# Kernel optimization log

Hardware: AMD Instinct MI355X
Metric: run time of the kernel (lower is better)

The kernel has to match this reference:

```python
import jax, jax.numpy as jnp
import numpy as np

N_HEAD = 16

def setup_inputs() -> dict:
    key = jax.random.key(0)
    k1, k2, k3 = jax.random.split(key, 3)
    B, S, D = 2, 2048, 1024
    std = 0.02
    return {
        "hidden_states": jax.random.normal(k1, (B, S, D), jnp.float32),
        "w_attn": jax.random.normal(k2, (D, 3 * D), jnp.float32) * std,
        "b_attn": jnp.zeros((3 * D,), jnp.float32),
        "w_proj": jax.random.normal(k3, (D, D), jnp.float32) * std,
        "b_proj": jnp.zeros((D,), jnp.float32),
    }

def reference(hidden_states, w_attn, b_attn, w_proj, b_proj):
    B, S, D = hidden_states.shape
    H = N_HEAD
    hd = D // H
    # fused qkv projection (Conv1D == x @ W + b)
    qkv = hidden_states @ w_attn + b_attn            # [B,S,3D]
    q, k, v = jnp.split(qkv, 3, axis=-1)
    def split_heads(t):
        return t.reshape(B, S, H, hd).transpose(0, 2, 1, 3)  # [B,H,S,hd]
    q, k, v = split_heads(q), split_heads(k), split_heads(v)
    # scores with scale = sqrt(head_dim)
    scores = jnp.einsum('bhqd,bhkd->bhqk', q, k) / jnp.sqrt(jnp.asarray(hd, q.dtype))
    causal = jnp.tril(jnp.ones((S, S), bool))
    mask_value = jnp.finfo(scores.dtype).min
    scores = jnp.where(causal, scores, mask_value)
    attn = jax.nn.softmax(scores, axis=-1)           # dropout p=0 (eval)
    out = jnp.einsum('bhqk,bhkd->bhqd', attn, v)     # [B,H,S,hd]
    out = out.transpose(0, 2, 1, 3).reshape(B, S, D)
    out = out @ w_proj + b_proj
    return out
```

## Files before the change

### kernel.cpp

```cpp
#include <hip/hip_runtime.h>

#define S_LEN 2048
#define D_MODEL 1024
#define NHEAD 16
#define HDIM 64
#define BATCH 2
#define M_ROWS (BATCH * S_LEN)
#define N_QKV (3 * D_MODEL)
#define QSCALE 0.18033688011112042f

typedef __attribute__((ext_vector_type(8))) short bf16x8;
typedef __attribute__((ext_vector_type(4))) float f32x4;

static __device__ __forceinline__ unsigned short f2bf(float f) {
  unsigned int u = __float_as_uint(f);
  u += 0x7FFFu + ((u >> 16) & 1u);
  return (unsigned short)(u >> 16);
}
static __device__ __forceinline__ unsigned int pkbf(float a, float b) {
  unsigned int ua = __float_as_uint(a) + 0x8000u;
  unsigned int ub = __float_as_uint(b) + 0x8000u;
  return __builtin_amdgcn_perm(ub, ua, 0x07060302u);
}

static __device__ __forceinline__ void async_cp16(unsigned short* lds, const unsigned short* g) {
  __builtin_amdgcn_global_load_lds((__attribute__((address_space(1))) void*)g,
                                   (__attribute__((address_space(3))) void*)lds, 16, 0, 0);
}

__global__ __launch_bounds__(256) void k_prep(const float* __restrict__ x,
                                              unsigned short* __restrict__ xb,
                                              const float* __restrict__ w_attn,
                                              unsigned short* __restrict__ wqkvT,
                                              const float* __restrict__ w_proj,
                                              unsigned short* __restrict__ wprojT) {
  __shared__ unsigned short T[32][33];
  const int blk = blockIdx.x;
  const int tid = threadIdx.x;
  if (blk < 4096) {
    int i = blk * 256 + tid;
    float4 v = ((const float4*)x)[i];
    ushort4 o;
    o.x = f2bf(v.x); o.y = f2bf(v.y); o.z = f2bf(v.z); o.w = f2bf(v.w);
    ((ushort4*)xb)[i] = o;
    return;
  }
  const float* w;
  unsigned short* wT;
  int bid, Ndim;
  if (blk < 7168) { bid = blk - 4096; w = w_attn; wT = wqkvT; Ndim = N_QKV; }
  else            { bid = blk - 7168; w = w_proj; wT = wprojT; Ndim = D_MODEL; }
  const int nb = Ndim / 32;
  const int n0 = (bid % nb) * 32, k0 = (bid / nb) * 32;
  const int tx = tid & 31, ty = tid >> 5;
#pragma unroll
  for (int j = 0; j < 4; ++j) {
    int r = ty + j * 8;
    T[r][tx] = f2bf(w[(size_t)(k0 + r) * Ndim + n0 + tx]);
  }
  __syncthreads();
#pragma unroll
  for (int j = 0; j < 4; ++j) {
    int r = ty + j * 8;
    wT[(size_t)(n0 + r) * D_MODEL + k0 + tx] = T[tx][r];
  }
}

__global__ __launch_bounds__(256) void k_gemm_qkv(const unsigned short* __restrict__ A,
                                                  const unsigned short* __restrict__ Bt,
                                                  const float* __restrict__ bias,
                                                  unsigned short* __restrict__ Qb,
                                                  unsigned short* __restrict__ Kbuf,
                                                  unsigned short* __restrict__ VTb) {
  __shared__ __align__(16) unsigned short As[2][128 * 32];
  __shared__ __align__(16) unsigned short Bs[2][128 * 32];
  const int tid = threadIdx.x;
  const int wid = tid >> 6, lane = tid & 63;
  const int lr = lane & 15, lg = lane >> 4;
  const int blk = blockIdx.x;
  const int xcd = blk & 7, idx = blk >> 3;
  const int bm = ((xcd & 3) * 8 + (idx & 7)) * 128;
  const int bn = ((xcd >> 2) * 12 + (idx >> 3)) * 128;
  const int wm = (wid >> 1) * 64, wn = (wid & 1) * 64;
  const int K = D_MODEL;
  const int c0 = tid, c1 = tid + 256;
  const size_t a0o = (size_t)(bm + (c0 >> 2)) * K + (c0 & 3) * 8;
  const size_t a1o = (size_t)(bm + (c1 >> 2)) * K + (c1 & 3) * 8;
  const size_t b0o = (size_t)(bn + (c0 >> 2)) * K + (c0 & 3) * 8;
  const size_t b1o = (size_t)(bn + (c1 >> 2)) * K + (c1 & 3) * 8;

  f32x4 acc[4][4] = {};

  async_cp16(&As[0][c0 * 8], &A[a0o]);
  async_cp16(&As[0][c1 * 8], &A[a1o]);
  async_cp16(&Bs[0][c0 * 8], &Bt[b0o]);
  async_cp16(&Bs[0][c1 * 8], &Bt[b1o]);

  for (int k0 = 0; k0 < K; k0 += 32) {
    const int p = (k0 >> 5) & 1;
    __syncthreads();
    if (k0 + 32 < K) {
      async_cp16(&As[p ^ 1][c0 * 8], &A[a0o + k0 + 32]);
      async_cp16(&As[p ^ 1][c1 * 8], &A[a1o + k0 + 32]);
      async_cp16(&Bs[p ^ 1][c0 * 8], &Bt[b0o + k0 + 32]);
      async_cp16(&Bs[p ^ 1][c1 * 8], &Bt[b1o + k0 + 32]);
    }
    bf16x8 af[4], bfr[4];
#pragma unroll
    for (int i = 0; i < 4; ++i) af[i] = *(const bf16x8*)&As[p][(wm + i * 16 + lr) * 32 + lg * 8];
#pragma unroll
    for (int t = 0; t < 4; ++t) bfr[t] = *(const bf16x8*)&Bs[p][(wn + t * 16 + lr) * 32 + lg * 8];
#pragma unroll
    for (int i = 0; i < 4; ++i)
#pragma unroll
      for (int t = 0; t < 4; ++t)
        acc[i][t] = __builtin_amdgcn_mfma_f32_16x16x32_bf16(af[i], bfr[t], acc[i][t], 0, 0, 0);
  }
#pragma unroll
  for (int i = 0; i < 4; ++i) {
#pragma unroll
    for (int t = 0; t < 4; ++t) {
      int n = bn + wn + t * 16 + lr;
      int part = n >> 10, rem = n & 1023;
      int h = rem >> 6, d = rem & 63;
      float bv = bias[n];
      int row0 = bm + wm + i * 16 + lg * 4;
      int bb = row0 >> 11, s0 = row0 & 2047;
      if (part == 2) {
        ushort4 vv;
        vv.x = f2bf(acc[i][t][0] + bv);
        vv.y = f2bf(acc[i][t][1] + bv);
        vv.z = f2bf(acc[i][t][2] + bv);
        vv.w = f2bf(acc[i][t][3] + bv);
        *(ushort4*)&VTb[(((size_t)(bb << 4) + h) * HDIM + d) * S_LEN + s0] = vv;
      } else {
        unsigned short* dst = (part == 0) ? Qb : Kbuf;
        float sc = (part == 0) ? QSCALE : 1.0f;
#pragma unroll
        for (int r = 0; r < 4; ++r)
          dst[(((size_t)(bb << 4) + h) * S_LEN + (s0 + r)) * HDIM + d] = f2bf((acc[i][t][r] + bv) * sc);
      }
    }
  }
}

__global__ __launch_bounds__(256) void k_gemm_proj(const unsigned short* __restrict__ A,
                                                   const unsigned short* __restrict__ Bt,
                                                   const float* __restrict__ bias,
                                                   float* __restrict__ out) {
  __shared__ __align__(16) unsigned short As[2][128 * 32];
  __shared__ __align__(16) unsigned short Bs[2][128 * 32];
  const int tid = threadIdx.x;
  const int wid = tid >> 6, lane = tid & 63;
  const int lr = lane & 15, lg = lane >> 4;
  const int blk = blockIdx.x;
  const int xcd = blk & 7, idx = blk >> 3;
  const int bm = (xcd * 4 + (idx & 3)) * 128;
  const int bn = (idx >> 2) * 128;
  const int wm = (wid >> 1) * 64, wn = (wid & 1) * 64;
  const int K = D_MODEL;
  const int c0 = tid, c1 = tid + 256;
  const size_t a0o = (size_t)(bm + (c0 >> 2)) * K + (c0 & 3) * 8;
  const size_t a1o = (size_t)(bm + (c1 >> 2)) * K + (c1 & 3) * 8;
  const size_t b0o = (size_t)(bn + (c0 >> 2)) * K + (c0 & 3) * 8;
  const size_t b1o = (size_t)(bn + (c1 >> 2)) * K + (c1 & 3) * 8;

  f32x4 acc[4][4] = {};

  async_cp16(&As[0][c0 * 8], &A[a0o]);
  async_cp16(&As[0][c1 * 8], &A[a1o]);
  async_cp16(&Bs[0][c0 * 8], &Bt[b0o]);
  async_cp16(&Bs[0][c1 * 8], &Bt[b1o]);

  for (int k0 = 0; k0 < K; k0 += 32) {
    const int p = (k0 >> 5) & 1;
    __syncthreads();
    if (k0 + 32 < K) {
      async_cp16(&As[p ^ 1][c0 * 8], &A[a0o + k0 + 32]);
      async_cp16(&As[p ^ 1][c1 * 8], &A[a1o + k0 + 32]);
      async_cp16(&Bs[p ^ 1][c0 * 8], &Bt[b0o + k0 + 32]);
      async_cp16(&Bs[p ^ 1][c1 * 8], &Bt[b1o + k0 + 32]);
    }
    bf16x8 af[4], bfr[4];
#pragma unroll
    for (int i = 0; i < 4; ++i) af[i] = *(const bf16x8*)&As[p][(wm + i * 16 + lr) * 32 + lg * 8];
#pragma unroll
    for (int t = 0; t < 4; ++t) bfr[t] = *(const bf16x8*)&Bs[p][(wn + t * 16 + lr) * 32 + lg * 8];
#pragma unroll
    for (int i = 0; i < 4; ++i)
#pragma unroll
      for (int t = 0; t < 4; ++t)
        acc[i][t] = __builtin_amdgcn_mfma_f32_16x16x32_bf16(af[i], bfr[t], acc[i][t], 0, 0, 0);
  }
#pragma unroll
  for (int i = 0; i < 4; ++i) {
#pragma unroll
    for (int t = 0; t < 4; ++t) {
      int n = bn + wn + t * 16 + lr;
      float bv = bias[n];
#pragma unroll
      for (int r = 0; r < 4; ++r) {
        int row = bm + wm + i * 16 + lg * 4 + r;
        out[(size_t)row * D_MODEL + n] = acc[i][t][r] + bv;
      }
    }
  }
}

__global__ __launch_bounds__(256, 2) void k_attn6(const unsigned short* __restrict__ Qb,
                                                  const unsigned short* __restrict__ Kb,
                                                  const unsigned short* __restrict__ VT,
                                                  unsigned short* __restrict__ AO) {
  const int tid = threadIdx.x;
  const int wid = tid >> 6, lane = tid & 63;
  const int lr = lane & 15, quad = lane >> 4;
  const int bh = blockIdx.x;
  const int slot = blockIdx.y;
  const int b = bh >> 4, h = bh & 15;

  __shared__ __align__(16) unsigned short Ks[64 * 64];
  __shared__ __align__(16) unsigned short Vs[64 * 64];
  __shared__ __align__(16) unsigned short Pbuf[4][16 * 72];
  unsigned short* pb = &Pbuf[wid][0];

  const unsigned short* Kbh = Kb + (size_t)bh * S_LEN * HDIM;
  const unsigned short* VTbh = VT + (size_t)bh * HDIM * S_LEN;

  const int sL = slot * 4 + wid;
  const int Rs[2] = {sL * 16, (127 - sL) * 16};
  const int ntile = ((127 - slot * 4) >> 2) + 1;

  bf16x8 qf[2][2];
#pragma unroll
  for (int st = 0; st < 2; ++st)
#pragma unroll
    for (int dh = 0; dh < 2; ++dh)
      qf[st][dh] = *(const bf16x8*)&Qb[((size_t)bh * S_LEN + Rs[st] + lr) * HDIM + dh * 32 + quad * 8];

  f32x4 Ot[2][4] = {};
  float ms[2] = {-1e30f, -1e30f};
  float ls[2] = {0.f, 0.f};

  const int srow = lane >> 3;
  const int scol = ((lane & 7) ^ srow) * 8;

  for (int kt = 0; kt < ntile; ++kt) {
    const int k0 = kt * 64;
    __syncthreads();
#pragma unroll
    for (int j = 0; j < 2; ++j) {
      const int r0 = wid * 16 + j * 8;
      async_cp16(&Ks[r0 * 64 + lane * 8], &Kbh[(size_t)(k0 + r0 + srow) * HDIM + scol]);
      async_cp16(&Vs[r0 * 64 + lane * 8], &VTbh[(size_t)(r0 + srow) * S_LEN + k0 + scol]);
    }
    __syncthreads();

    bf16x8 kf[4][2], vf[4][2];
#pragma unroll
    for (int kg = 0; kg < 4; ++kg)
#pragma unroll
      for (int dh = 0; dh < 2; ++dh)
        kf[kg][dh] = *(const bf16x8*)&Ks[(kg * 16 + lr) * 64 + (((dh * 4 + quad) ^ (lr & 7)) * 8)];
#pragma unroll
    for (int dg = 0; dg < 4; ++dg)
#pragma unroll
      for (int kh = 0; kh < 2; ++kh)
        vf[dg][kh] = *(const bf16x8*)&Vs[(dg * 16 + lr) * 64 + (((kh * 4 + quad) ^ (lr & 7)) * 8)];

#pragma unroll
    for (int st = 0; st < 2; ++st) {
      const int R = Rs[st];
      if (k0 > R + 15) continue;
      f32x4 Sv[4];
#pragma unroll
      for (int kg = 0; kg < 4; ++kg) {
        f32x4 a = {};
        a = __builtin_amdgcn_mfma_f32_16x16x32_bf16(kf[kg][0], qf[st][0], a, 0, 0, 0);
        a = __builtin_amdgcn_mfma_f32_16x16x32_bf16(kf[kg][1], qf[st][1], a, 0, 0, 0);
        Sv[kg] = a;
      }
      if (k0 + 63 > R) {
        const int q = R + lr;
#pragma unroll
        for (int kg = 0; kg < 4; ++kg)
#pragma unroll
          for (int r = 0; r < 4; ++r)
            if (k0 + kg * 16 + quad * 4 + r > q) Sv[kg][r] = -1e30f;
      }
      float mx = ms[st];
#pragma unroll
      for (int kg = 0; kg < 4; ++kg)
        mx = fmaxf(mx, fmaxf(fmaxf(Sv[kg][0], Sv[kg][1]), fmaxf(Sv[kg][2], Sv[kg][3])));
      mx = fmaxf(mx, __shfl_xor(mx, 16));
      mx = fmaxf(mx, __shfl_xor(mx, 32));
      const float alpha = __builtin_amdgcn_exp2f(ms[st] - mx);
      ms[st] = mx;
      float rs = 0.f;
#pragma unroll
      for (int kg = 0; kg < 4; ++kg) {
        float e0 = __builtin_amdgcn_exp2f(Sv[kg][0] - mx);
        float e1 = __builtin_amdgcn_exp2f(Sv[kg][1] - mx);
        float e2 = __builtin_amdgcn_exp2f(Sv[kg][2] - mx);
        float e3 = __builtin_amdgcn_exp2f(Sv[kg][3] - mx);
        rs += (e0 + e1) + (e2 + e3);
        *(unsigned int*)&pb[lr * 72 + kg * 16 + quad * 4]     = pkbf(e0, e1);
        *(unsigned int*)&pb[lr * 72 + kg * 16 + quad * 4 + 2] = pkbf(e2, e3);
      }
      rs += __shfl_xor(rs, 16);
      rs += __shfl_xor(rs, 32);
      ls[st] = ls[st] * alpha + rs;
#pragma unroll
      for (int dg = 0; dg < 4; ++dg)
#pragma unroll
        for (int r = 0; r < 4; ++r) Ot[st][dg][r] *= alpha;
      bf16x8 pf0 = *(const bf16x8*)&pb[lr * 72 + quad * 8];
      bf16x8 pf1 = *(const bf16x8*)&pb[lr * 72 + 32 + quad * 8];
#pragma unroll
      for (int dg = 0; dg < 4; ++dg) {
        Ot[st][dg] = __builtin_amdgcn_mfma_f32_16x16x32_bf16(vf[dg][0], pf0, Ot[st][dg], 0, 0, 0);
        Ot[st][dg] = __builtin_amdgcn_mfma_f32_16x16x32_bf16(vf[dg][1], pf1, Ot[st][dg], 0, 0, 0);
      }
    }
  }

#pragma unroll
  for (int st = 0; st < 2; ++st) {
    const float rl = __builtin_amdgcn_rcpf(ls[st]);
    const int s = Rs[st] + lr;
#pragma unroll
    for (int dg = 0; dg < 4; ++dg) {
      const size_t o = ((size_t)b * S_LEN + s) * D_MODEL + h * 64 + dg * 16 + quad * 4;
      *(unsigned int*)&AO[o]     = pkbf(Ot[st][dg][0] * rl, Ot[st][dg][1] * rl);
      *(unsigned int*)&AO[o + 2] = pkbf(Ot[st][dg][2] * rl, Ot[st][dg][3] * rl);
    }
  }
}

extern "C" void kernel_launch(void* const* d_in, const int* in_sizes, int n_in,
                              void* d_out, int out_size, void* d_ws, size_t ws_size,
                              hipStream_t stream) {
  const float* x      = (const float*)d_in[0];
  const float* w_attn = (const float*)d_in[1];
  const float* b_attn = (const float*)d_in[2];
  const float* w_proj = (const float*)d_in[3];
  const float* b_proj = (const float*)d_in[4];
  float* out = (float*)d_out;

  unsigned short* ws     = (unsigned short*)d_ws;
  unsigned short* xb     = ws;
  unsigned short* wqkvT  = xb + (size_t)M_ROWS * D_MODEL;
  unsigned short* wprojT = wqkvT + (size_t)N_QKV * D_MODEL;
  unsigned short* Qb     = wprojT + (size_t)D_MODEL * D_MODEL;
  unsigned short* Kb     = Qb + (size_t)M_ROWS * D_MODEL;
  unsigned short* VT     = Kb + (size_t)M_ROWS * D_MODEL;
  unsigned short* AO     = xb;

  k_prep<<<8192, 256, 0, stream>>>(x, xb, w_attn, wqkvT, w_proj, wprojT);
  k_gemm_qkv<<<768, 256, 0, stream>>>(xb, wqkvT, b_attn, Qb, Kb, VT);
  k_attn6<<<dim3(BATCH * NHEAD, 16), 256, 0, stream>>>(Qb, Kb, VT, AO);
  k_gemm_proj<<<256, 256, 0, stream>>>(AO, wprojT, b_proj, out);
}
```

Baseline: 179.9 us.

## Double-buffer K/V tiles in attention and flatten grid with reordered slots

The attention kernel now keeps two LDS buffers for the K and V tiles. It prefetches the next tile with async copies while computing on the current one, replacing the load-then-barrier pattern that stalled each iteration. The 2D grid becomes a 1D grid, with the work-slot order reversed for the second half of blocks, to change how uneven causal work is scheduled across CUs. LDS use per block roughly doubles for K/V. Overlap depends on the compiler not inserting conservative waits on the outstanding LDS-targeted loads.

```diff
diff --git a/kernel.cpp b/kernel.cpp
--- a/kernel.cpp
+++ b/kernel.cpp
@@ -207,19 +207,21 @@
   }
 }
 
-__global__ __launch_bounds__(256, 2) void k_attn6(const unsigned short* __restrict__ Qb,
+__global__ __launch_bounds__(256, 2) void k_attn7(const unsigned short* __restrict__ Qb,
                                                   const unsigned short* __restrict__ Kb,
                                                   const unsigned short* __restrict__ VT,
                                                   unsigned short* __restrict__ AO) {
   const int tid = threadIdx.x;
   const int wid = tid >> 6, lane = tid & 63;
   const int lr = lane & 15, quad = lane >> 4;
-  const int bh = blockIdx.x;
-  const int slot = blockIdx.y;
+  const int blk = blockIdx.x;
+  const int bh = blk & 31;
+  const int g = blk >> 5;
+  const int slot = (g < 8) ? g : 23 - g;
   const int b = bh >> 4, h = bh & 15;
 
-  __shared__ __align__(16) unsigned short Ks[64 * 64];
-  __shared__ __align__(16) unsigned short Vs[64 * 64];
+  __shared__ __align__(16) unsigned short Ks[2][64 * 64];
+  __shared__ __align__(16) unsigned short Vs[2][64 * 64];
   __shared__ __align__(16) unsigned short Pbuf[4][16 * 72];
   unsigned short* pb = &Pbuf[wid][0];
 
@@ -244,28 +246,38 @@
   const int srow = lane >> 3;
   const int scol = ((lane & 7) ^ srow) * 8;
 
+#pragma unroll
+  for (int j = 0; j < 2; ++j) {
+    const int r0 = wid * 16 + j * 8;
+    async_cp16(&Ks[0][r0 * 64 + lane * 8], &Kbh[(size_t)(r0 + srow) * HDIM + scol]);
+    async_cp16(&Vs[0][r0 * 64 + lane * 8], &VTbh[(size_t)(r0 + srow) * S_LEN + scol]);
+  }
+
   for (int kt = 0; kt < ntile; ++kt) {
     const int k0 = kt * 64;
+    const int p = kt & 1;
     __syncthreads();
-#pragma unroll
-    for (int j = 0; j < 2; ++j) {
-      const int r0 = wid * 16 + j * 8;
-      async_cp16(&Ks[r0 * 64 + lane * 8], &Kbh[(size_t)(k0 + r0 + srow) * HDIM + scol]);
-      async_cp16(&Vs[r0 * 64 + lane * 8], &VTbh[(size_t)(r0 + srow) * S_LEN + k0 + scol]);
-    }
-    __syncthreads();
+    if (kt + 1 < ntile) {
+      const int kn = k0 + 64;
+#pragma unroll
+      for (int j = 0; j < 2; ++j) {
+        const int r0 = wid * 16 + j * 8;
+        async_cp16(&Ks[p ^ 1][r0 * 64 + lane * 8], &Kbh[(size_t)(kn + r0 + srow) * HDIM + scol]);
+        async_cp16(&Vs[p ^ 1][r0 * 64 + lane * 8], &VTbh[(size_t)(r0 + srow) * S_LEN + kn + scol]);
+      }
+    }
 
     bf16x8 kf[4][2], vf[4][2];
 #pragma unroll
     for (int kg = 0; kg < 4; ++kg)
 #pragma unroll
       for (int dh = 0; dh < 2; ++dh)
-        kf[kg][dh] = *(const bf16x8*)&Ks[(kg * 16 + lr) * 64 + (((dh * 4 + quad) ^ (lr & 7)) * 8)];
+        kf[kg][dh] = *(const bf16x8*)&Ks[p][(kg * 16 + lr) * 64 + (((dh * 4 + quad) ^ (lr & 7)) * 8)];
 #pragma unroll
     for (int dg = 0; dg < 4; ++dg)
 #pragma unroll
       for (int kh = 0; kh < 2; ++kh)
-        vf[dg][kh] = *(const bf16x8*)&Vs[(dg * 16 + lr) * 64 + (((kh * 4 + quad) ^ (lr & 7)) * 8)];
+        vf[dg][kh] = *(const bf16x8*)&Vs[p][(dg * 16 + lr) * 64 + (((kh * 4 + quad) ^ (lr & 7)) * 8)];
 
 #pragma unroll
     for (int st = 0; st < 2; ++st) {
@@ -357,6 +369,6 @@
 
   k_prep<<<8192, 256, 0, stream>>>(x, xb, w_attn, wqkvT, w_proj, wprojT);
   k_gemm_qkv<<<768, 256, 0, stream>>>(xb, wqkvT, b_attn, Qb, Kb, VT);
-  k_attn6<<<dim3(BATCH * NHEAD, 16), 256, 0, stream>>>(Qb, Kb, VT, AO);
+  k_attn7<<<512, 256, 0, stream>>>(Qb, Kb, VT, AO);
   k_gemm_proj<<<256, 256, 0, stream>>>(AO, wprojT, b_proj, out);
 }
```

Result: no change. 179.7 us (-0.1%).

## Use 128-key attention tiles, reorder block schedule, and halve proj GEMM N-tile

Applied to the files above, without the earlier changes.

The attention kernel now processes 128 keys per loop iteration, loading a 128-row K tile and two 64-wide V halves. This halves the number of barrier/load rounds, and the fully masked second half is skipped near the diagonal. The grid is flattened to 512 blocks with a slot ordering that pairs light and heavy causal slots. The projection GEMM switches to 128x64 tiles and 512 blocks to fill more CUs. The costs are more LDS and register use in attention, V fragments reloaded from LDS per query stripe, and some loops no longer unrolled.

```diff
diff --git a/kernel.cpp b/kernel.cpp
--- a/kernel.cpp
+++ b/kernel.cpp
@@ -149,28 +149,26 @@
                                                    const float* __restrict__ bias,
                                                    float* __restrict__ out) {
   __shared__ __align__(16) unsigned short As[2][128 * 32];
-  __shared__ __align__(16) unsigned short Bs[2][128 * 32];
+  __shared__ __align__(16) unsigned short Bs[2][64 * 32];
   const int tid = threadIdx.x;
   const int wid = tid >> 6, lane = tid & 63;
   const int lr = lane & 15, lg = lane >> 4;
   const int blk = blockIdx.x;
   const int xcd = blk & 7, idx = blk >> 3;
   const int bm = (xcd * 4 + (idx & 3)) * 128;
-  const int bn = (idx >> 2) * 128;
-  const int wm = (wid >> 1) * 64, wn = (wid & 1) * 64;
+  const int bn = (idx >> 2) * 64;
+  const int wm = (wid >> 1) * 64, wn = (wid & 1) * 32;
   const int K = D_MODEL;
   const int c0 = tid, c1 = tid + 256;
   const size_t a0o = (size_t)(bm + (c0 >> 2)) * K + (c0 & 3) * 8;
   const size_t a1o = (size_t)(bm + (c1 >> 2)) * K + (c1 & 3) * 8;
   const size_t b0o = (size_t)(bn + (c0 >> 2)) * K + (c0 & 3) * 8;
-  const size_t b1o = (size_t)(bn + (c1 >> 2)) * K + (c1 & 3) * 8;
-
-  f32x4 acc[4][4] = {};
+
+  f32x4 acc[4][2] = {};
 
   async_cp16(&As[0][c0 * 8], &A[a0o]);
   async_cp16(&As[0][c1 * 8], &A[a1o]);
   async_cp16(&Bs[0][c0 * 8], &Bt[b0o]);
-  async_cp16(&Bs[0][c1 * 8], &Bt[b1o]);
 
   for (int k0 = 0; k0 < K; k0 += 32) {
     const int p = (k0 >> 5) & 1;
@@ -179,23 +177,22 @@
       async_cp16(&As[p ^ 1][c0 * 8], &A[a0o + k0 + 32]);
       async_cp16(&As[p ^ 1][c1 * 8], &A[a1o + k0 + 32]);
       async_cp16(&Bs[p ^ 1][c0 * 8], &Bt[b0o + k0 + 32]);
-      async_cp16(&Bs[p ^ 1][c1 * 8], &Bt[b1o + k0 + 32]);
-    }
-    bf16x8 af[4], bfr[4];
+    }
+    bf16x8 af[4], bfr[2];
 #pragma unroll
     for (int i = 0; i < 4; ++i) af[i] = *(const bf16x8*)&As[p][(wm + i * 16 + lr) * 32 + lg * 8];
 #pragma unroll
-    for (int t = 0; t < 4; ++t) bfr[t] = *(const bf16x8*)&Bs[p][(wn + t * 16 + lr) * 32 + lg * 8];
+    for (int t = 0; t < 2; ++t) bfr[t] = *(const bf16x8*)&Bs[p][(wn + t * 16 + lr) * 32 + lg * 8];
 #pragma unroll
     for (int i = 0; i < 4; ++i)
 #pragma unroll
-      for (int t = 0; t < 4; ++t)
+      for (int t = 0; t < 2; ++t)
         acc[i][t] = __builtin_amdgcn_mfma_f32_16x16x32_bf16(af[i], bfr[t], acc[i][t], 0, 0, 0);
   }
 #pragma unroll
   for (int i = 0; i < 4; ++i) {
 #pragma unroll
-    for (int t = 0; t < 4; ++t) {
+    for (int t = 0; t < 2; ++t) {
       int n = bn + wn + t * 16 + lr;
       float bv = bias[n];
 #pragma unroll
@@ -207,20 +204,22 @@
   }
 }
 
-__global__ __launch_bounds__(256, 2) void k_attn6(const unsigned short* __restrict__ Qb,
+__global__ __launch_bounds__(256, 2) void k_attn9(const unsigned short* __restrict__ Qb,
                                                   const unsigned short* __restrict__ Kb,
                                                   const unsigned short* __restrict__ VT,
                                                   unsigned short* __restrict__ AO) {
   const int tid = threadIdx.x;
   const int wid = tid >> 6, lane = tid & 63;
   const int lr = lane & 15, quad = lane >> 4;
-  const int bh = blockIdx.x;
-  const int slot = blockIdx.y;
+  const int blk = blockIdx.x;
+  const int bh = blk & 31;
+  const int g = blk >> 5;
+  const int slot = (g < 8) ? g : 23 - g;
   const int b = bh >> 4, h = bh & 15;
 
-  __shared__ __align__(16) unsigned short Ks[64 * 64];
-  __shared__ __align__(16) unsigned short Vs[64 * 64];
-  __shared__ __align__(16) unsigned short Pbuf[4][16 * 72];
+  __shared__ __align__(16) unsigned short Ks[128 * 64];
+  __shared__ __align__(16) unsigned short Vs[2][64 * 64];
+  __shared__ __align__(16) unsigned short Pbuf[4][16 * 136];
   unsigned short* pb = &Pbuf[wid][0];
 
   const unsigned short* Kbh = Kb + (size_t)bh * S_LEN * HDIM;
@@ -228,7 +227,8 @@
 
   const int sL = slot * 4 + wid;
   const int Rs[2] = {sL * 16, (127 - sL) * 16};
-  const int ntile = ((127 - slot * 4) >> 2) + 1;
+  const int ntile = 32 - slot;
+  const int nsup = (ntile + 1) >> 1;
 
   bf16x8 qf[2][2];
 #pragma unroll
@@ -244,34 +244,37 @@
   const int srow = lane >> 3;
   const int scol = ((lane & 7) ^ srow) * 8;
 
-  for (int kt = 0; kt < ntile; ++kt) {
-    const int k0 = kt * 64;
+  for (int sp = 0; sp < nsup; ++sp) {
+    const int k0 = sp * 128;
     __syncthreads();
 #pragma unroll
-    for (int j = 0; j < 2; ++j) {
-      const int r0 = wid * 16 + j * 8;
+    for (int j = 0; j < 4; ++j) {
+      const int r0 = wid * 32 + j * 8;
       async_cp16(&Ks[r0 * 64 + lane * 8], &Kbh[(size_t)(k0 + r0 + srow) * HDIM + scol]);
-      async_cp16(&Vs[r0 * 64 + lane * 8], &VTbh[(size_t)(r0 + srow) * S_LEN + k0 + scol]);
-    }
+    }
+#pragma unroll
+    for (int hf = 0; hf < 2; ++hf)
+#pragma unroll
+      for (int j = 0; j < 2; ++j) {
+        const int r0 = wid * 16 + j * 8;
+        async_cp16(&Vs[hf][r0 * 64 + lane * 8],
+                   &VTbh[(size_t)(r0 + srow) * S_LEN + k0 + hf * 64 + scol]);
+      }
     __syncthreads();
 
-    bf16x8 kf[4][2], vf[4][2];
-#pragma unroll
-    for (int kg = 0; kg < 4; ++kg)
+    bf16x8 kf[8][2];
+#pragma unroll
+    for (int kg = 0; kg < 8; ++kg)
 #pragma unroll
       for (int dh = 0; dh < 2; ++dh)
         kf[kg][dh] = *(const bf16x8*)&Ks[(kg * 16 + lr) * 64 + (((dh * 4 + quad) ^ (lr & 7)) * 8)];
-#pragma unroll
-    for (int dg = 0; dg < 4; ++dg)
-#pragma unroll
-      for (int kh = 0; kh < 2; ++kh)
-        vf[dg][kh] = *(const bf16x8*)&Vs[(dg * 16 + lr) * 64 + (((kh * 4 + quad) ^ (lr & 7)) * 8)];
 
 #pragma unroll
     for (int st = 0; st < 2; ++st) {
       const int R = Rs[st];
       if (k0 > R + 15) continue;
-      f32x4 Sv[4];
+      const bool v1 = (k0 + 64 <= R + 15);
+      f32x4 Sv[8];
 #pragma unroll
       for (int kg = 0; kg < 4; ++kg) {
         f32x4 a = {};
@@ -279,32 +282,39 @@
         a = __builtin_amdgcn_mfma_f32_16x16x32_bf16(kf[kg][1], qf[st][1], a, 0, 0, 0);
         Sv[kg] = a;
       }
-      if (k0 + 63 > R) {
+      if (v1) {
+#pragma unroll
+        for (int kg = 4; kg < 8; ++kg) {
+          f32x4 a = {};
+          a = __builtin_amdgcn_mfma_f32_16x16x32_bf16(kf[kg][0], qf[st][0], a, 0, 0, 0);
+          a = __builtin_amdgcn_mfma_f32_16x16x32_bf16(kf[kg][1], qf[st][1], a, 0, 0, 0);
+          Sv[kg] = a;
+        }
+      }
+      const int nkg = v1 ? 8 : 4;
+      if (k0 + 127 > R) {
         const int q = R + lr;
-#pragma unroll
-        for (int kg = 0; kg < 4; ++kg)
+        for (int kg = 0; kg < nkg; ++kg)
 #pragma unroll
           for (int r = 0; r < 4; ++r)
             if (k0 + kg * 16 + quad * 4 + r > q) Sv[kg][r] = -1e30f;
       }
       float mx = ms[st];
-#pragma unroll
-      for (int kg = 0; kg < 4; ++kg)
+      for (int kg = 0; kg < nkg; ++kg)
         mx = fmaxf(mx, fmaxf(fmaxf(Sv[kg][0], Sv[kg][1]), fmaxf(Sv[kg][2], Sv[kg][3])));
       mx = fmaxf(mx, __shfl_xor(mx, 16));
       mx = fmaxf(mx, __shfl_xor(mx, 32));
       const float alpha = __builtin_amdgcn_exp2f(ms[st] - mx);
       ms[st] = mx;
       float rs = 0.f;
-#pragma unroll
-      for (int kg = 0; kg < 4; ++kg) {
+      for (int kg = 0; kg < nkg; ++kg) {
         float e0 = __builtin_amdgcn_exp2f(Sv[kg][0] - mx);
         float e1 = __builtin_amdgcn_exp2f(Sv[kg][1] - mx);
         float e2 = __builtin_amdgcn_exp2f(Sv[kg][2] - mx);
         float e3 = __builtin_amdgcn_exp2f(Sv[kg][3] - mx);
         rs += (e0 + e1) + (e2 + e3);
-        *(unsigned int*)&pb[lr * 72 + kg * 16 + quad * 4]     = pkbf(e0, e1);
-        *(unsigned int*)&pb[lr * 72 + kg * 16 + quad * 4 + 2] = pkbf(e2, e3);
+        *(unsigned int*)&pb[lr * 136 + kg * 16 + quad * 4]     = pkbf(e0, e1);
+        *(unsigned int*)&pb[lr * 136 + kg * 16 + quad * 4 + 2] = pkbf(e2, e3);
       }
       rs += __shfl_xor(rs, 16);
       rs += __shfl_xor(rs, 32);
@@ -313,12 +323,17 @@
       for (int dg = 0; dg < 4; ++dg)
 #pragma unroll
         for (int r = 0; r < 4; ++r) Ot[st][dg][r] *= alpha;
-      bf16x8 pf0 = *(const bf16x8*)&pb[lr * 72 + quad * 8];
-      bf16x8 pf1 = *(const bf16x8*)&pb[lr * 72 + 32 + quad * 8];
-#pragma unroll
-      for (int dg = 0; dg < 4; ++dg) {
-        Ot[st][dg] = __builtin_amdgcn_mfma_f32_16x16x32_bf16(vf[dg][0], pf0, Ot[st][dg], 0, 0, 0);
-        Ot[st][dg] = __builtin_amdgcn_mfma_f32_16x16x32_bf16(vf[dg][1], pf1, Ot[st][dg], 0, 0, 0);
+      for (int hf = 0; hf < (v1 ? 2 : 1); ++hf) {
+        bf16x8 pf0 = *(const bf16x8*)&pb[lr * 136 + hf * 64 + quad * 8];
+        bf16x8 pf1 = *(const bf16x8*)&pb[lr * 136 + hf * 64 + 32 + quad * 8];
+#pragma unroll
+        for (int dg = 0; dg < 4; ++dg) {
+          const int vr = (dg * 16 + lr) * 64;
+          bf16x8 vf0 = *(const bf16x8*)&Vs[hf][vr + ((quad ^ (lr & 7)) * 8)];
+          bf16x8 vf1 = *(const bf16x8*)&Vs[hf][vr + (((4 + quad) ^ (lr & 7)) * 8)];
+          Ot[st][dg] = __builtin_amdgcn_mfma_f32_16x16x32_bf16(vf0, pf0, Ot[st][dg], 0, 0, 0);
+          Ot[st][dg] = __builtin_amdgcn_mfma_f32_16x16x32_bf16(vf1, pf1, Ot[st][dg], 0, 0, 0);
+        }
       }
     }
   }
@@ -357,6 +372,6 @@
 
   k_prep<<<8192, 256, 0, stream>>>(x, xb, w_attn, wqkvT, w_proj, wprojT);
   k_gemm_qkv<<<768, 256, 0, stream>>>(xb, wqkvT, b_attn, Qb, Kb, VT);
-  k_attn6<<<dim3(BATCH * NHEAD, 16), 256, 0, stream>>>(Qb, Kb, VT, AO);
-  k_gemm_proj<<<256, 256, 0, stream>>>(AO, wprojT, b_proj, out);
-}
+  k_attn9<<<512, 256, 0, stream>>>(Qb, Kb, VT, AO);
+  k_gemm_proj<<<512, 256, 0, stream>>>(AO, wprojT, b_proj, out);
+}
```

New measurement: 195.1 us. +8.4%, slower.
